# Kernel optimization log

Measured on AMD Instinct MI355X. Metric: run time of the kernel, lower is better.

Reference implementation:

```python
import jax, jax.numpy as jnp
import numpy as np

B = 65536
E = 1024      # embedding_dim
NC = 8        # num_chunks
CD = E // NC  # chunk_dim = 128
H = 2         # num_heads
QK = 32       # qk_dim
VD = 64       # v_dim
LN_EPS = 1e-5


def _sinusoidal_pe():
    pos = np.arange(NC, dtype=np.float32)[:, None]
    div = np.exp(np.arange(0, CD, 2, dtype=np.float32) * (-np.log(10000.0) / CD))
    pe = np.zeros((NC, CD), dtype=np.float32)
    pe[:, 0::2] = np.sin(pos * div)
    pe[:, 1::2] = np.cos(pos * div)
    return jnp.asarray(pe)


def _rel_index():
    c = np.arange(NC)
    return jnp.asarray(c[None, :] - c[:, None] + (NC - 1))  # [NC, NC] in [0, 2*NC-2]


def setup_inputs() -> dict:
    key = jax.random.key(0)
    ks = jax.random.split(key, 6)
    x = jax.random.normal(ks[0], (B, E), dtype=jnp.float32)
    Wq = jax.random.normal(ks[1], (H * QK, CD), dtype=jnp.float32) * 0.02
    Wk = jax.random.normal(ks[2], (H * QK, CD), dtype=jnp.float32) * 0.02
    Wv = jax.random.normal(ks[3], (H * VD, CD), dtype=jnp.float32) * 0.02
    Wo = jax.random.normal(ks[4], (CD, H * VD), dtype=jnp.float32) * 0.02
    gamma = jnp.ones((CD,), dtype=jnp.float32)
    beta = jnp.zeros((CD,), dtype=jnp.float32)
    # relative_pos_bias init: bias[:, i] = -0.5 * |i - (NC-1)|
    dist = np.abs(np.arange(2 * NC - 1) - (NC - 1)).astype(np.float32)
    rel_bias = jnp.broadcast_to(jnp.asarray(-0.5 * dist), (H, 2 * NC - 1)).copy()
    return {"x": x, "Wq": Wq, "Wk": Wk, "Wv": Wv, "Wo": Wo,
            "gamma": gamma, "beta": beta, "rel_bias": rel_bias}


def reference(x, Wq, Wk, Wv, Wo, gamma, beta, rel_bias):
    pe = _sinusoidal_pe()           # [NC, CD]
    idx = _rel_index()              # [NC, NC] int
    scale = QK ** -0.5

    xc = x.reshape(-1, NC, CD) + pe[None]                     # [B, NC, CD]
    Q = (xc @ Wq.T).reshape(-1, NC, H, QK).transpose(0, 2, 1, 3)  # [B,H,NC,QK]
    K = (xc @ Wk.T).reshape(-1, NC, H, QK).transpose(0, 2, 1, 3)
    V = (xc @ Wv.T).reshape(-1, NC, H, VD).transpose(0, 2, 1, 3)  # [B,H,NC,VD]

    scores = jnp.einsum('bhnq,bhmq->bhnm', Q, K) * scale          # [B,H,NC,NC]
    scores = scores + rel_bias[:, idx][None]                      # gathered rel-pos bias
    attn = jax.nn.softmax(scores, axis=-1)                        # dropout = identity (eval)

    ctx = jnp.einsum('bhnm,bhmv->bhnv', attn, V)                  # [B,H,NC,VD]
    ctx = ctx.transpose(0, 2, 1, 3).reshape(-1, NC, H * VD)       # [B,NC,H*VD]
    out = ctx @ Wo.T                                              # [B,NC,CD]

    h = xc + out
    mu = jnp.mean(h, axis=-1, keepdims=True)
    var = jnp.var(h, axis=-1, keepdims=True)
    y = (h - mu) * jax.lax.rsqrt(var + LN_EPS) * gamma + beta
    return y.reshape(-1, E), attn
```

## Files before the change

kernel.cpp:

```cpp
#include <hip/hip_runtime.h>

typedef __attribute__((ext_vector_type(8))) short bf16x8;
typedef __attribute__((ext_vector_type(4))) float f32x4;
typedef __attribute__((ext_vector_type(2))) unsigned int u32x2;

union UB8 { bf16x8 v; unsigned d[4]; unsigned short u[8]; };

__device__ __forceinline__ float bf2f(unsigned short u) {
  union { unsigned u; float f; } a; a.u = ((unsigned)u) << 16;
  return a.f;
}
__device__ __forceinline__ unsigned pk2bf(float lo, float hi) {
  union { __bf16 b[2]; unsigned u; } r;
  r.b[0] = (__bf16)lo; r.b[1] = (__bf16)hi;
  return r.u;
}
__device__ __forceinline__ unsigned short f2bf(float f) {
  union { float f; unsigned u; } a; a.f = f;
  return (unsigned short)((a.u + 0x7fffu + ((a.u >> 16) & 1u)) >> 16);
}

__global__ void prep_kernel(const float* __restrict__ Wq, const float* __restrict__ Wk,
                            const float* __restrict__ Wv, const float* __restrict__ Wo,
                            unsigned short* __restrict__ ws) {
  const int b = blockIdx.x;
  if (b < 192) {
    int i = b * 256 + threadIdx.x;
    float v;
    if (i < 8192) v = Wq[i];
    else if (i < 16384) v = Wk[i - 8192];
    else if (i < 32768) v = Wv[i - 16384];
    else v = Wo[i - 32768];
    ws[i] = f2bf(v);
  } else {
    float* pe = (float*)(ws + 49152);
#pragma unroll
    for (int k = 0; k < 4; ++k) {
      int e = threadIdx.x * 4 + k;
      int c = e >> 7, col = e & 127;
      float div = expf(-0.14391156831212727f * (float)(col >> 1));
      float ang = (float)c * div;
      pe[e] = (col & 1) ? cosf(ang) : sinf(ang);
    }
  }
}

__global__ __launch_bounds__(256, 3)
void wlmha_kernel(const float* __restrict__ x,
                  const unsigned short* __restrict__ wA,
                  const unsigned short* __restrict__ wOb,
                  const float* __restrict__ peG,
                  const float* __restrict__ gamma,
                  const float* __restrict__ beta,
                  const float* __restrict__ relb,
                  float* __restrict__ y_out,
                  float* __restrict__ attn_out)
{
  const int t   = threadIdx.x;
  const int l   = t & 63;
  const int w   = t >> 6;
  const int c   = l & 15;
  const int kg  = l >> 4;
  const int mr0 = t >> 4;
  const int cgf = t & 15;
  const int sw0 = (mr0 & 15) << 4;
  const int qc  = l & 7;
  const long b0 = (long)blockIdx.x * 8;

  __shared__ __align__(16) char smem[32768];
  char* xcS = smem;
  char* qkS = smem + 16384;

  const float* xb = x + b0 * 1024;
  f32x4 xg[4][2];
#pragma unroll
  for (int i = 0; i < 4; ++i) {
    const float* p = xb + (t + 256 * i) * 8;
    xg[i][0] = *(const f32x4*)p;
    xg[i][1] = *(const f32x4*)(p + 4);
  }
  const float* per = peG + (mr0 & 7) * 128 + cgf * 8;
  const f32x4 pe0 = *(const f32x4*)per;
  const f32x4 pe1 = *(const f32x4*)(per + 4);

  float bias[4];
#pragma unroll
  for (int j = 0; j < 4; ++j)
    bias[j] = relb[(w & 1) * 15 + (kg & 1) * 4 + j - qc + 7];

  bf16x8 wf[4][4];
#pragma unroll
  for (int nb = 0; nb < 4; ++nb) {
    const unsigned short* src = wA + (w * 64 + nb * 16 + c) * 128 + kg * 8;
#pragma unroll
    for (int ks = 0; ks < 4; ++ks) wf[nb][ks] = *(const bf16x8*)(src + ks * 32);
  }

#pragma unroll
  for (int i = 0; i < 4; ++i) {
    const int m = mr0 + 16 * i;
    f32x4 a0 = xg[i][0] + pe0;
    f32x4 a1 = xg[i][1] + pe1;
    UB8 fr;
    fr.d[0] = pk2bf(a0[0], a0[1]); fr.d[1] = pk2bf(a0[2], a0[3]);
    fr.d[2] = pk2bf(a1[0], a1[1]); fr.d[3] = pk2bf(a1[2], a1[3]);
    *(bf16x8*)(xcS + m * 256 + ((cgf * 16) ^ sw0)) = fr.v;
  }
  __syncthreads();

  unsigned vv[4][4][2];
#pragma unroll
  for (int mt = 0; mt < 4; ++mt) {
    bf16x8 xf[4];
    const int row = mt * 16 + c;
    const int rsw = (row & 15) << 4;
#pragma unroll
    for (int ks = 0; ks < 4; ++ks)
      xf[ks] = *(const bf16x8*)(xcS + row * 256 + ((ks * 64 + kg * 16) ^ rsw));
    if (w < 2) {
#pragma unroll
      for (int nb = 0; nb < 4; ++nb) {
        f32x4 acc = {0.f, 0.f, 0.f, 0.f};
#pragma unroll
        for (int ks = 0; ks < 4; ++ks)
          acc = __builtin_amdgcn_mfma_f32_16x16x32_bf16(wf[nb][ks], xf[ks], acc, 0, 0, 0);
        u32x2 pk; pk.x = pk2bf(acc[0], acc[1]); pk.y = pk2bf(acc[2], acc[3]);
        const int colb = (w * 128 + nb * 32 + kg * 8) ^ rsw;
        *(u32x2*)(qkS + row * 256 + colb) = pk;
      }
    } else {
#pragma unroll
      for (int nb = 0; nb < 4; ++nb) {
        f32x4 acc = {0.f, 0.f, 0.f, 0.f};
#pragma unroll
        for (int ks = 0; ks < 4; ++ks)
          acc = __builtin_amdgcn_mfma_f32_16x16x32_bf16(xf[ks], wf[nb][ks], acc, 0, 0, 0);
        vv[nb][mt][0] = pk2bf(acc[0], acc[1]);
        vv[nb][mt][1] = pk2bf(acc[2], acc[3]);
      }
    }
  }
  bf16x8 xcr[4];
#pragma unroll
  for (int i = 0; i < 4; ++i)
    xcr[i] = *(const bf16x8*)(xcS + (mr0 + 16 * i) * 256 + ((cgf * 16) ^ sw0));
  __syncthreads();

  bf16x8 wof[2][4];
#pragma unroll
  for (int nt = 0; nt < 2; ++nt) {
    const unsigned short* src = wOb + (w * 32 + nt * 16 + c) * 128 + kg * 8;
#pragma unroll
    for (int ks = 0; ks < 4; ++ks) wof[nt][ks] = *(const bf16x8*)(src + ks * 32);
  }
  {
    const int h = w & 1;
    const bool vmask = ((l >> 5) & 1) == ((l >> 3) & 1);
    const int sA = c + ((kg & 1) << 5);
    const f32x4 zero = {0.f, 0.f, 0.f, 0.f};
#pragma unroll
    for (int T = 0; T < 4; ++T) {
      const int row = T * 16 + c;
      const int sw = (row & 15) << 4;
      bf16x8 kf = *(const bf16x8*)(qkS + row * 256 + ((128 + h * 64 + kg * 16) ^ sw));
      bf16x8 qf = *(const bf16x8*)(qkS + row * 256 + ((h * 64 + kg * 16) ^ sw));
      f32x4 st = __builtin_amdgcn_mfma_f32_16x16x32_bf16(kf, qf, zero, 0, 0, 0);
      float s0[4];
#pragma unroll
      for (int j = 0; j < 4; ++j)
        s0[j] = vmask ? st[j] * 0.17677669529663687f + bias[j] : -1e30f;
      float mx = fmaxf(fmaxf(s0[0], s0[1]), fmaxf(s0[2], s0[3]));
      mx = fmaxf(mx, __shfl_xor(mx, 16));
      mx = fmaxf(mx, __shfl_xor(mx, 32));
      float p[4], sum = 0.f;
#pragma unroll
      for (int j = 0; j < 4; ++j) { p[j] = __expf(s0[j] - mx); sum += p[j]; }
      sum += __shfl_xor(sum, 16);
      sum += __shfl_xor(sum, 32);
      const float inv = 1.0f / sum;
#pragma unroll
      for (int j = 0; j < 4; ++j) p[j] *= inv;

      if (w < 2) {
        if (vmask) {
          float* ap = attn_out + ((b0 + (row >> 3)) * 2 + h) * 64 + qc * 8 + (kg & 1) * 4;
          const f32x4 pv = {p[0], p[1], p[2], p[3]};
          *(f32x4*)ap = pv;
        }
      } else {
        const unsigned P0 = pk2bf(p[0], p[1]);
        const unsigned P1 = pk2bf(p[2], p[3]);
        UB8 pf;
        pf.d[0] = (unsigned)__shfl((int)P0, sA);
        pf.d[1] = (unsigned)__shfl((int)P1, sA);
        pf.d[2] = (unsigned)__shfl((int)P0, sA + 16);
        pf.d[3] = (unsigned)__shfl((int)P1, sA + 16);
        if (kg >= 2) { pf.d[0] = 0; pf.d[1] = 0; pf.d[2] = 0; pf.d[3] = 0; }
#pragma unroll
        for (int nb = 0; nb < 4; ++nb) {
          UB8 vt;
          vt.d[0] = (unsigned)__shfl((int)vv[nb][T][0], sA);
          vt.d[1] = (unsigned)__shfl((int)vv[nb][T][1], sA);
          vt.d[2] = (unsigned)__shfl((int)vv[nb][T][0], sA + 16);
          vt.d[3] = (unsigned)__shfl((int)vv[nb][T][1], sA + 16);
          if (kg >= 2) { vt.d[0] = 0; vt.d[1] = 0; vt.d[2] = 0; vt.d[3] = 0; }
          const f32x4 cacc = __builtin_amdgcn_mfma_f32_16x16x32_bf16(vt.v, pf.v, zero, 0, 0, 0);
          u32x2 pk; pk.x = pk2bf(cacc[0], cacc[1]); pk.y = pk2bf(cacc[2], cacc[3]);
          const int fb = ((w - 2) * 128 + nb * 32 + kg * 8) ^ sw;
          *(u32x2*)(xcS + row * 256 + fb) = pk;
        }
      }
    }
  }
  __syncthreads();

#pragma unroll
  for (int mt = 0; mt < 4; ++mt) {
    bf16x8 cf[4];
    const int row = mt * 16 + c;
    const int rsw = (row & 15) << 4;
#pragma unroll
    for (int ks = 0; ks < 4; ++ks)
      cf[ks] = *(const bf16x8*)(xcS + row * 256 + ((ks * 64 + kg * 16) ^ rsw));
#pragma unroll
    for (int nt = 0; nt < 2; ++nt) {
      f32x4 acc = {0.f, 0.f, 0.f, 0.f};
#pragma unroll
      for (int ks = 0; ks < 4; ++ks)
        acc = __builtin_amdgcn_mfma_f32_16x16x32_bf16(wof[nt][ks], cf[ks], acc, 0, 0, 0);
      u32x2 pk; pk.x = pk2bf(acc[0], acc[1]); pk.y = pk2bf(acc[2], acc[3]);
      const int colb = (w * 64 + nt * 32 + kg * 8) ^ rsw;
      *(u32x2*)(qkS + row * 256 + colb) = pk;
    }
  }
  __syncthreads();

  {
    const f32x4 gm0 = *(const f32x4*)(gamma + cgf * 8);
    const f32x4 gm1 = *(const f32x4*)(gamma + cgf * 8 + 4);
    const f32x4 bt0 = *(const f32x4*)(beta + cgf * 8);
    const f32x4 bt1 = *(const f32x4*)(beta + cgf * 8 + 4);
    float* yb = y_out + b0 * 1024;
#pragma unroll
    for (int i = 0; i < 4; ++i) {
      const int m = mr0 + 16 * i;
      UB8 hh; hh.v = *(const bf16x8*)(qkS + m * 256 + ((cgf * 16) ^ sw0));
      UB8 xr; xr.v = xcr[i];
      float hv[8];
      float sum = 0.f, sq = 0.f;
#pragma unroll
      for (int j = 0; j < 8; ++j) {
        hv[j] = bf2f(hh.u[j]) + bf2f(xr.u[j]);
        sum += hv[j]; sq += hv[j] * hv[j];
      }
#pragma unroll
      for (int d = 1; d < 16; d <<= 1) {
        sum += __shfl_xor(sum, d);
        sq  += __shfl_xor(sq, d);
      }
      const float mu = sum * 0.0078125f;
      const float rs = rsqrtf(sq * 0.0078125f - mu * mu + 1e-5f);
      f32x4 o0, o1;
#pragma unroll
      for (int j = 0; j < 4; ++j) {
        o0[j] = (hv[j]     - mu) * rs * gm0[j] + bt0[j];
        o1[j] = (hv[4 + j] - mu) * rs * gm1[j] + bt1[j];
      }
      const int g = t + 256 * i;
      *(f32x4*)(yb + g * 8) = o0;
      *(f32x4*)(yb + g * 8 + 4) = o1;
    }
  }
}

extern "C" void kernel_launch(void* const* d_in, const int* in_sizes, int n_in,
                              void* d_out, int out_size, void* d_ws, size_t ws_size,
                              hipStream_t stream) {
  (void)in_sizes; (void)n_in; (void)out_size; (void)ws_size;
  const float* x    = (const float*)d_in[0];
  const float* Wq   = (const float*)d_in[1];
  const float* Wk   = (const float*)d_in[2];
  const float* Wv   = (const float*)d_in[3];
  const float* Wo   = (const float*)d_in[4];
  const float* gam  = (const float*)d_in[5];
  const float* bet  = (const float*)d_in[6];
  const float* relb = (const float*)d_in[7];
  float* y    = (float*)d_out;
  float* attn = y + (size_t)65536 * 1024;
  unsigned short* ws = (unsigned short*)d_ws;
  const float* peG = (const float*)(ws + 49152);

  hipLaunchKernelGGL(prep_kernel, dim3(193), dim3(256), 0, stream, Wq, Wk, Wv, Wo, ws);
  hipLaunchKernelGGL(wlmha_kernel, dim3(8192), dim3(256), 0, stream,
                     x, ws, ws + 32768, peG, gam, bet, relb, y, attn);
}
```

Before: 177.0 us.

## Balance QKV work across all waves and fuse residual and LayerNorm into Wo epilogue

Before, waves 0-1 computed Q/K and waves 2-3 computed V, then the work split again by role. Now every wave computes half a Q/K slice and half a V slice, and all four waves run softmax and P·V for one head. This balances MFMA work and removes divergent branches. The Wo projection adds the residual and computes LayerNorm partial sums in registers, exchanged through a small shared buffer, so the bf16 round-trip of h through LDS is gone. Output writes now go by 16-float row segments instead of contiguous 8-float chunks per thread, which may change coalescing. Softmax is also computed redundantly by two waves per head.

```diff
diff --git a/kernel.cpp b/kernel.cpp
--- a/kernel.cpp
+++ b/kernel.cpp
@@ -2,6 +2,7 @@
 
 typedef __attribute__((ext_vector_type(8))) short bf16x8;
 typedef __attribute__((ext_vector_type(4))) float f32x4;
+typedef __attribute__((ext_vector_type(2))) float f32x2;
 typedef __attribute__((ext_vector_type(2))) unsigned int u32x2;
 
 union UB8 { bf16x8 v; unsigned d[4]; unsigned short u[8]; };
@@ -63,8 +64,9 @@
   const int kg  = l >> 4;
   const int mr0 = t >> 4;
   const int cgf = t & 15;
-  const int sw0 = (mr0 & 15) << 4;
-  const int qc  = l & 7;
+  const int sw0 = mr0 << 4;
+  const int qc  = c & 7;
+  const int rsw = c << 4;
   const long b0 = (long)blockIdx.x * 8;
 
   __shared__ __align__(16) char smem[32768];
@@ -83,17 +85,22 @@
   const f32x4 pe0 = *(const f32x4*)per;
   const f32x4 pe1 = *(const f32x4*)(per + 4);
 
+  const int h2 = w >> 1;
   float bias[4];
 #pragma unroll
   for (int j = 0; j < 4; ++j)
-    bias[j] = relb[(w & 1) * 15 + (kg & 1) * 4 + j - qc + 7];
-
-  bf16x8 wf[4][4];
-#pragma unroll
-  for (int nb = 0; nb < 4; ++nb) {
-    const unsigned short* src = wA + (w * 64 + nb * 16 + c) * 128 + kg * 8;
-#pragma unroll
-    for (int ks = 0; ks < 4; ++ks) wf[nb][ks] = *(const bf16x8*)(src + ks * 32);
+    bias[j] = relb[h2 * 15 + (kg & 1) * 4 + j - qc + 7];
+
+  bf16x8 wf[2][4], wv[2][4];
+#pragma unroll
+  for (int nb = 0; nb < 2; ++nb) {
+    const unsigned short* sQK = wA + (w * 32 + nb * 16 + c) * 128 + kg * 8;
+    const unsigned short* sV  = wA + (128 + w * 32 + nb * 16 + c) * 128 + kg * 8;
+#pragma unroll
+    for (int ks = 0; ks < 4; ++ks) {
+      wf[nb][ks] = *(const bf16x8*)(sQK + ks * 32);
+      wv[nb][ks] = *(const bf16x8*)(sV + ks * 32);
+    }
   }
 
 #pragma unroll
@@ -108,42 +115,41 @@
   }
   __syncthreads();
 
-  unsigned vv[4][4][2];
+  unsigned vv[2][4][2];
 #pragma unroll
   for (int mt = 0; mt < 4; ++mt) {
     bf16x8 xf[4];
     const int row = mt * 16 + c;
-    const int rsw = (row & 15) << 4;
 #pragma unroll
     for (int ks = 0; ks < 4; ++ks)
       xf[ks] = *(const bf16x8*)(xcS + row * 256 + ((ks * 64 + kg * 16) ^ rsw));
-    if (w < 2) {
-#pragma unroll
-      for (int nb = 0; nb < 4; ++nb) {
-        f32x4 acc = {0.f, 0.f, 0.f, 0.f};
-#pragma unroll
-        for (int ks = 0; ks < 4; ++ks)
-          acc = __builtin_amdgcn_mfma_f32_16x16x32_bf16(wf[nb][ks], xf[ks], acc, 0, 0, 0);
-        u32x2 pk; pk.x = pk2bf(acc[0], acc[1]); pk.y = pk2bf(acc[2], acc[3]);
-        const int colb = (w * 128 + nb * 32 + kg * 8) ^ rsw;
-        *(u32x2*)(qkS + row * 256 + colb) = pk;
-      }
-    } else {
-#pragma unroll
-      for (int nb = 0; nb < 4; ++nb) {
-        f32x4 acc = {0.f, 0.f, 0.f, 0.f};
-#pragma unroll
-        for (int ks = 0; ks < 4; ++ks)
-          acc = __builtin_amdgcn_mfma_f32_16x16x32_bf16(xf[ks], wf[nb][ks], acc, 0, 0, 0);
-        vv[nb][mt][0] = pk2bf(acc[0], acc[1]);
-        vv[nb][mt][1] = pk2bf(acc[2], acc[3]);
-      }
-    }
-  }
-  bf16x8 xcr[4];
-#pragma unroll
-  for (int i = 0; i < 4; ++i)
-    xcr[i] = *(const bf16x8*)(xcS + (mr0 + 16 * i) * 256 + ((cgf * 16) ^ sw0));
+#pragma unroll
+    for (int nb = 0; nb < 2; ++nb) {
+      f32x4 acc = {0.f, 0.f, 0.f, 0.f};
+#pragma unroll
+      for (int ks = 0; ks < 4; ++ks)
+        acc = __builtin_amdgcn_mfma_f32_16x16x32_bf16(wf[nb][ks], xf[ks], acc, 0, 0, 0);
+      u32x2 pk; pk.x = pk2bf(acc[0], acc[1]); pk.y = pk2bf(acc[2], acc[3]);
+      *(u32x2*)(qkS + row * 256 + ((w * 64 + nb * 32 + kg * 8) ^ rsw)) = pk;
+    }
+#pragma unroll
+    for (int nb = 0; nb < 2; ++nb) {
+      f32x4 acc = {0.f, 0.f, 0.f, 0.f};
+#pragma unroll
+      for (int ks = 0; ks < 4; ++ks)
+        acc = __builtin_amdgcn_mfma_f32_16x16x32_bf16(xf[ks], wv[nb][ks], acc, 0, 0, 0);
+      vv[nb][mt][0] = pk2bf(acc[0], acc[1]);
+      vv[nb][mt][1] = pk2bf(acc[2], acc[3]);
+    }
+  }
+  unsigned xr[4][2][2];
+#pragma unroll
+  for (int mt = 0; mt < 4; ++mt)
+#pragma unroll
+    for (int nt = 0; nt < 2; ++nt) {
+      u32x2 rr = *(const u32x2*)(xcS + (mt * 16 + c) * 256 + ((w * 64 + nt * 32 + kg * 8) ^ rsw));
+      xr[mt][nt][0] = rr.x; xr[mt][nt][1] = rr.y;
+    }
   __syncthreads();
 
   bf16x8 wof[2][4];
@@ -153,17 +159,21 @@
 #pragma unroll
     for (int ks = 0; ks < 4; ++ks) wof[nt][ks] = *(const bf16x8*)(src + ks * 32);
   }
+  f32x4 gm[2], bt[2];
+#pragma unroll
+  for (int nt = 0; nt < 2; ++nt) {
+    gm[nt] = *(const f32x4*)(gamma + w * 32 + nt * 16 + kg * 4);
+    bt[nt] = *(const f32x4*)(beta  + w * 32 + nt * 16 + kg * 4);
+  }
   {
-    const int h = w & 1;
     const bool vmask = ((l >> 5) & 1) == ((l >> 3) & 1);
     const int sA = c + ((kg & 1) << 5);
     const f32x4 zero = {0.f, 0.f, 0.f, 0.f};
 #pragma unroll
     for (int T = 0; T < 4; ++T) {
       const int row = T * 16 + c;
-      const int sw = (row & 15) << 4;
-      bf16x8 kf = *(const bf16x8*)(qkS + row * 256 + ((128 + h * 64 + kg * 16) ^ sw));
-      bf16x8 qf = *(const bf16x8*)(qkS + row * 256 + ((h * 64 + kg * 16) ^ sw));
+      bf16x8 kf = *(const bf16x8*)(qkS + row * 256 + ((128 + h2 * 64 + kg * 16) ^ rsw));
+      bf16x8 qf = *(const bf16x8*)(qkS + row * 256 + ((h2 * 64 + kg * 16) ^ rsw));
       f32x4 st = __builtin_amdgcn_mfma_f32_16x16x32_bf16(kf, qf, zero, 0, 0, 0);
       float s0[4];
 #pragma unroll
@@ -181,94 +191,88 @@
 #pragma unroll
       for (int j = 0; j < 4; ++j) p[j] *= inv;
 
-      if (w < 2) {
-        if (vmask) {
-          float* ap = attn_out + ((b0 + (row >> 3)) * 2 + h) * 64 + qc * 8 + (kg & 1) * 4;
-          const f32x4 pv = {p[0], p[1], p[2], p[3]};
-          *(f32x4*)ap = pv;
-        }
-      } else {
-        const unsigned P0 = pk2bf(p[0], p[1]);
-        const unsigned P1 = pk2bf(p[2], p[3]);
-        UB8 pf;
-        pf.d[0] = (unsigned)__shfl((int)P0, sA);
-        pf.d[1] = (unsigned)__shfl((int)P1, sA);
-        pf.d[2] = (unsigned)__shfl((int)P0, sA + 16);
-        pf.d[3] = (unsigned)__shfl((int)P1, sA + 16);
-        if (kg >= 2) { pf.d[0] = 0; pf.d[1] = 0; pf.d[2] = 0; pf.d[3] = 0; }
-#pragma unroll
-        for (int nb = 0; nb < 4; ++nb) {
-          UB8 vt;
-          vt.d[0] = (unsigned)__shfl((int)vv[nb][T][0], sA);
-          vt.d[1] = (unsigned)__shfl((int)vv[nb][T][1], sA);
-          vt.d[2] = (unsigned)__shfl((int)vv[nb][T][0], sA + 16);
-          vt.d[3] = (unsigned)__shfl((int)vv[nb][T][1], sA + 16);
-          if (kg >= 2) { vt.d[0] = 0; vt.d[1] = 0; vt.d[2] = 0; vt.d[3] = 0; }
-          const f32x4 cacc = __builtin_amdgcn_mfma_f32_16x16x32_bf16(vt.v, pf.v, zero, 0, 0, 0);
-          u32x2 pk; pk.x = pk2bf(cacc[0], cacc[1]); pk.y = pk2bf(cacc[2], cacc[3]);
-          const int fb = ((w - 2) * 128 + nb * 32 + kg * 8) ^ sw;
-          *(u32x2*)(xcS + row * 256 + fb) = pk;
-        }
+      if ((w & 1) == 0 && vmask) {
+        float* ap = attn_out + ((b0 + (row >> 3)) * 2 + h2) * 64 + qc * 8 + (kg & 1) * 4;
+        const f32x4 pv = {p[0], p[1], p[2], p[3]};
+        *(f32x4*)ap = pv;
       }
+
+      const unsigned P0 = pk2bf(p[0], p[1]);
+      const unsigned P1 = pk2bf(p[2], p[3]);
+      UB8 pf;
+      pf.d[0] = (unsigned)__shfl((int)P0, sA);
+      pf.d[1] = (unsigned)__shfl((int)P1, sA);
+      pf.d[2] = (unsigned)__shfl((int)P0, sA + 16);
+      pf.d[3] = (unsigned)__shfl((int)P1, sA + 16);
+      if (kg >= 2) { pf.d[0] = 0; pf.d[1] = 0; pf.d[2] = 0; pf.d[3] = 0; }
+
+#pragma unroll
+      for (int nb = 0; nb < 2; ++nb) {
+        UB8 vt;
+        vt.d[0] = (unsigned)__shfl((int)vv[nb][T][0], sA);
+        vt.d[1] = (unsigned)__shfl((int)vv[nb][T][1], sA);
+        vt.d[2] = (unsigned)__shfl((int)vv[nb][T][0], sA + 16);
+        vt.d[3] = (unsigned)__shfl((int)vv[nb][T][1], sA + 16);
+        if (kg >= 2) { vt.d[0] = 0; vt.d[1] = 0; vt.d[2] = 0; vt.d[3] = 0; }
+        const f32x4 cacc = __builtin_amdgcn_mfma_f32_16x16x32_bf16(vt.v, pf.v, zero, 0, 0, 0);
+        u32x2 pk; pk.x = pk2bf(cacc[0], cacc[1]); pk.y = pk2bf(cacc[2], cacc[3]);
+        *(u32x2*)(xcS + row * 256 + ((w * 64 + nb * 32 + kg * 8) ^ rsw)) = pk;
+      }
     }
   }
   __syncthreads();
 
+  f32x4 hreg[4][2];
 #pragma unroll
   for (int mt = 0; mt < 4; ++mt) {
     bf16x8 cf[4];
     const int row = mt * 16 + c;
-    const int rsw = (row & 15) << 4;
 #pragma unroll
     for (int ks = 0; ks < 4; ++ks)
       cf[ks] = *(const bf16x8*)(xcS + row * 256 + ((ks * 64 + kg * 16) ^ rsw));
+    float s = 0.f, q = 0.f;
 #pragma unroll
     for (int nt = 0; nt < 2; ++nt) {
       f32x4 acc = {0.f, 0.f, 0.f, 0.f};
 #pragma unroll
       for (int ks = 0; ks < 4; ++ks)
         acc = __builtin_amdgcn_mfma_f32_16x16x32_bf16(wof[nt][ks], cf[ks], acc, 0, 0, 0);
-      u32x2 pk; pk.x = pk2bf(acc[0], acc[1]); pk.y = pk2bf(acc[2], acc[3]);
-      const int colb = (w * 64 + nt * 32 + kg * 8) ^ rsw;
-      *(u32x2*)(qkS + row * 256 + colb) = pk;
+      UB8 rr; rr.d[0] = xr[mt][nt][0]; rr.d[1] = xr[mt][nt][1];
+#pragma unroll
+      for (int j = 0; j < 4; ++j) {
+        acc[j] += bf2f(rr.u[j]);
+        s += acc[j]; q += acc[j] * acc[j];
+      }
+      hreg[mt][nt] = acc;
+    }
+    s += __shfl_xor(s, 16); q += __shfl_xor(q, 16);
+    s += __shfl_xor(s, 32); q += __shfl_xor(q, 32);
+    if (kg == 0) {
+      f32x2 pr; pr.x = s; pr.y = q;
+      *(f32x2*)(qkS + row * 32 + w * 8) = pr;
     }
   }
   __syncthreads();
 
   {
-    const f32x4 gm0 = *(const f32x4*)(gamma + cgf * 8);
-    const f32x4 gm1 = *(const f32x4*)(gamma + cgf * 8 + 4);
-    const f32x4 bt0 = *(const f32x4*)(beta + cgf * 8);
-    const f32x4 bt1 = *(const f32x4*)(beta + cgf * 8 + 4);
     float* yb = y_out + b0 * 1024;
 #pragma unroll
-    for (int i = 0; i < 4; ++i) {
-      const int m = mr0 + 16 * i;
-      UB8 hh; hh.v = *(const bf16x8*)(qkS + m * 256 + ((cgf * 16) ^ sw0));
-      UB8 xr; xr.v = xcr[i];
-      float hv[8];
-      float sum = 0.f, sq = 0.f;
-#pragma unroll
-      for (int j = 0; j < 8; ++j) {
-        hv[j] = bf2f(hh.u[j]) + bf2f(xr.u[j]);
-        sum += hv[j]; sq += hv[j] * hv[j];
+    for (int mt = 0; mt < 4; ++mt) {
+      const int row = mt * 16 + c;
+      const f32x4 sa = *(const f32x4*)(qkS + row * 32);
+      const f32x4 sb = *(const f32x4*)(qkS + row * 32 + 16);
+      const float s = sa[0] + sa[2] + sb[0] + sb[2];
+      const float q = sa[1] + sa[3] + sb[1] + sb[3];
+      const float mu = s * 0.0078125f;
+      const float rs = rsqrtf(q * 0.0078125f - mu * mu + 1e-5f);
+#pragma unroll
+      for (int nt = 0; nt < 2; ++nt) {
+        f32x4 o;
+#pragma unroll
+        for (int j = 0; j < 4; ++j)
+          o[j] = (hreg[mt][nt][j] - mu) * rs * gm[nt][j] + bt[nt][j];
+        *(f32x4*)(yb + row * 128 + w * 32 + nt * 16 + kg * 4) = o;
       }
-#pragma unroll
-      for (int d = 1; d < 16; d <<= 1) {
-        sum += __shfl_xor(sum, d);
-        sq  += __shfl_xor(sq, d);
-      }
-      const float mu = sum * 0.0078125f;
-      const float rs = rsqrtf(sq * 0.0078125f - mu * mu + 1e-5f);
-      f32x4 o0, o1;
-#pragma unroll
-      for (int j = 0; j < 4; ++j) {
-        o0[j] = (hv[j]     - mu) * rs * gm0[j] + bt0[j];
-        o1[j] = (hv[4 + j] - mu) * rs * gm1[j] + bt1[j];
-      }
-      const int g = t + 256 * i;
-      *(f32x4*)(yb + g * 8) = o0;
-      *(f32x4*)(yb + g * 8 + 4) = o1;
     }
   }
 }
```

Result: no change. 175.8 us (-0.7%).
